# Kernel optimization log

Hardware: AMD Instinct MI355X
Metric: run time of the kernel (lower is better)

Reference implementation:

```python
import jax, jax.numpy as jnp
import numpy as np

B, N_TOK, C = 64, 256, 1024
H = 16
PH, PW = 16, 16  # patch (window) size; N_TOK == PH*PW
D_FF = 4 * C
EPS = 1e-5


def rel_pos_idx(ph, pw):
    # Swin-style relative position index for a ph x pw window -> [ph*pw * ph*pw]
    coords_h = np.arange(ph)
    coords_w = np.arange(pw)
    coords = np.stack(np.meshgrid(coords_h, coords_w, indexing='ij'))  # [2, ph, pw]
    coords = coords.reshape(2, -1)  # [2, N]
    rel = coords[:, :, None] - coords[:, None, :]  # [2, N, N]
    rel = rel.transpose(1, 2, 0)  # [N, N, 2]
    rel[:, :, 0] += ph - 1
    rel[:, :, 1] += pw - 1
    rel[:, :, 0] *= 2 * pw - 1
    return rel.sum(-1).reshape(-1).astype(np.int32)  # [N*N]


def layernorm(x, g, b):
    mu = jnp.mean(x, axis=-1, keepdims=True)
    var = jnp.mean(jnp.square(x - mu), axis=-1, keepdims=True)
    return (x - mu) * jax.lax.rsqrt(var + EPS) * g + b


def setup_inputs() -> dict:
    key = jax.random.key(0)
    ks = jax.random.split(key, 12)
    s = lambda fan: 1.0 / np.sqrt(fan)
    inp = {
        'x': jax.random.normal(ks[0], (B, N_TOK, C), dtype=jnp.float32),
        'rel_pos_idx': jnp.asarray(rel_pos_idx(PH, PW)),
        'qkv_w': jax.random.normal(ks[1], (C, 3 * C), dtype=jnp.float32) * s(C),
        'qkv_b': jnp.zeros((3 * C,), dtype=jnp.float32),
        'proj_w': jax.random.normal(ks[2], (C, C), dtype=jnp.float32) * s(C),
        'proj_b': jnp.zeros((C,), dtype=jnp.float32),
        'rel_pos_bias': jax.random.uniform(ks[3], ((2 * PH - 1) * (2 * PW - 1), H), dtype=jnp.float32),
        'ln1_g': jnp.ones((C,), dtype=jnp.float32),
        'ln1_b': jnp.zeros((C,), dtype=jnp.float32),
        'ln2_g': jnp.ones((C,), dtype=jnp.float32),
        'ln2_b': jnp.zeros((C,), dtype=jnp.float32),
        'fc1_w': jax.random.normal(ks[4], (C, D_FF), dtype=jnp.float32) * s(C),
        'fc1_b': jnp.zeros((D_FF,), dtype=jnp.float32),
        'fc2_w': jax.random.normal(ks[5], (D_FF, C), dtype=jnp.float32) * s(D_FF),
        'fc2_b': jnp.zeros((C,), dtype=jnp.float32),
    }
    return inp


def reference(x, rel_pos_idx, qkv_w, qkv_b, proj_w, proj_b, rel_pos_bias,
              ln1_g, ln1_b, ln2_g, ln2_b, fc1_w, fc1_b, fc2_w, fc2_b):
    Bc, N, Cc = x.shape
    Dh = Cc // H
    scale = Dh ** -0.5

    # --- token mixer: RelAttention with pre-norm residual ---
    h = layernorm(x, ln1_g, ln1_b)
    qkv = (h @ qkv_w + qkv_b).reshape(Bc, N, 3, H, Dh)
    qkv = jnp.transpose(qkv, (2, 0, 3, 1, 4))  # [3, B, H, N, Dh]
    q, k, v = qkv[0] * scale, qkv[1], qkv[2]

    attn = jnp.einsum('bhnd,bhmd->bhnm', q, k)  # [B, H, N, N]
    # gathered relative position bias: [N*N] -> [N, N, H] -> [H, N, N]
    bias = rel_pos_bias[rel_pos_idx].reshape(N, N, H)
    attn = attn + jnp.transpose(bias, (2, 0, 1))[None]
    attn = jax.nn.softmax(attn, axis=-1)

    out = jnp.einsum('bhnm,bhmd->bhnd', attn, v)  # [B, H, N, Dh]
    out = jnp.transpose(out, (0, 2, 1, 3)).reshape(Bc, N, Cc)  # MergeHeads
    x = x + (out @ proj_w + proj_b)

    # --- MLP with pre-norm residual ---
    h2 = layernorm(x, ln2_g, ln2_b)
    h2 = jax.nn.gelu(h2 @ fc1_w + fc1_b)
    x = x + (h2 @ fc2_w + fc2_b)
    return x
```

## Files before the change

### kernel.cpp

```cpp
#include <hip/hip_runtime.h>
#include <hip/hip_bf16.h>
#include <math.h>

typedef __hip_bfloat16 bf16;
typedef __attribute__((ext_vector_type(8))) __bf16 bf16x8;
typedef __attribute__((ext_vector_type(4))) float f32x4;
typedef __attribute__((ext_vector_type(4))) unsigned u32x4;

#define NB 64
#define NTOK 256
#define CDIM 1024
#define NH 16
#define DH 64
#define DFF 4096
#define MROWS (NB * NTOK)

__device__ __forceinline__ float gelu_f(float x) {
    float t = 1.5957691216057308f * (x + 0.044715f * x * x * x);
    return x / (1.0f + __expf(-t));
}

__device__ __forceinline__ void gload_lds16(const void* g, void* l) {
    __builtin_amdgcn_global_load_lds((const __attribute__((address_space(1))) void*)g,
                                     (__attribute__((address_space(3))) void*)l,
                                     16, 0, 0);
}

__global__ void transpose_f32_bf16(const float* __restrict__ in, bf16* __restrict__ out,
                                   int R, int Cc) {
    __shared__ bf16 tile[32][33];
    int c0 = blockIdx.x * 32, r0 = blockIdx.y * 32;
    int t = threadIdx.x;
    int r = t >> 5, c = t & 31;
#pragma unroll
    for (int i = 0; i < 4; i++)
        tile[r + i * 8][c] = (bf16)in[(size_t)(r0 + r + i * 8) * Cc + c0 + c];
    __syncthreads();
#pragma unroll
    for (int i = 0; i < 4; i++)
        out[(size_t)(c0 + r + i * 8) * R + r0 + c] = tile[c][r + i * 8];
}

__global__ __launch_bounds__(256) void ln_kernel(const float* __restrict__ xin,
                                                 const float* __restrict__ g,
                                                 const float* __restrict__ b,
                                                 bf16* __restrict__ outp) {
    __shared__ float red[8];
    int row = blockIdx.x, t = threadIdx.x;
    float4 v = ((const float4*)(xin + (size_t)row * CDIM))[t];
    float s = v.x + v.y + v.z + v.w;
    float q = v.x * v.x + v.y * v.y + v.z * v.z + v.w * v.w;
#pragma unroll
    for (int off = 32; off > 0; off >>= 1) {
        s += __shfl_down(s, off);
        q += __shfl_down(q, off);
    }
    int wave = t >> 6;
    if ((t & 63) == 0) { red[wave] = s; red[4 + wave] = q; }
    __syncthreads();
    float st = red[0] + red[1] + red[2] + red[3];
    float qt = red[4] + red[5] + red[6] + red[7];
    float mu = st * (1.0f / CDIM);
    float rstd = rsqrtf(qt * (1.0f / CDIM) - mu * mu + 1e-5f);
    float4 gv = ((const float4*)g)[t];
    float4 bv = ((const float4*)b)[t];
    bf16* orow = outp + (size_t)row * CDIM + t * 4;
    orow[0] = (bf16)((v.x - mu) * rstd * gv.x + bv.x);
    orow[1] = (bf16)((v.y - mu) * rstd * gv.y + bv.y);
    orow[2] = (bf16)((v.z - mu) * rstd * gv.z + bv.z);
    orow[3] = (bf16)((v.w - mu) * rstd * gv.w + bv.w);
}

__global__ void biasq_kernel(const int* __restrict__ idx, const float* __restrict__ rpb,
                             float* __restrict__ bq) {
    int e = blockIdx.x * 256 + threadIdx.x;
    int k = e & 255, q = (e >> 8) & 255, h = e >> 16;
    bq[e] = rpb[idx[q * 256 + k] * NH + h];
}

__global__ __launch_bounds__(512, 2) void gemm_bt_kernel(
    const bf16* __restrict__ Abf, const bf16* __restrict__ Btbf,
    const float* __restrict__ bias, const float* resid,
    void* outp, size_t qstride, int M, int N, int K, int mode) {
    __shared__ __align__(16) u32x4 SL[4][2][1024];
    const unsigned short* A = (const unsigned short*)Abf;
    const unsigned short* Bt = (const unsigned short*)Btbf;
    int tid = threadIdx.x;
    int wave = tid >> 6, lane = tid & 63;
    int quad = lane >> 4, lr = lane & 15;
    int wm = (wave >> 2) << 7;
    int wn = (wave & 3) << 6;

    unsigned nx = gridDim.x;
    unsigned nwg = nx * gridDim.y;
    unsigned orig = blockIdx.y * nx + blockIdx.x;
    unsigned q8 = nwg >> 3, r8 = nwg & 7u;
    unsigned xcd = orig & 7u, io = orig >> 3;
    unsigned wg = (xcd < r8 ? xcd * (q8 + 1u) : r8 * (q8 + 1u) + (xcd - r8) * q8) + io;
    size_t row0 = (size_t)(wg / nx) << 8;
    size_t col0 = (size_t)(wg % nx) << 8;

    const unsigned short* Ag = A + row0 * K;
    const unsigned short* Bg = Bt + col0 * K;
    f32x4 acc[8][4] = {};

    const int wbase = tid & ~63;

    auto stage = [&](int s) {
        int slot = s & 3;
        int kbase = s << 5;
#pragma unroll
        for (int it = 0; it < 2; it++) {
            int ch = it * 512 + tid;
            int kk = ch >> 8, r = ch & 255;
            gload_lds16(Ag + (size_t)r * K + (kbase + kk * 8),
                        (void*)&SL[slot][0][it * 512 + wbase]);
        }
#pragma unroll
        for (int it = 0; it < 2; it++) {
            int ch = it * 512 + tid;
            int kk = ch >> 8, r = ch & 255;
            gload_lds16(Bg + (size_t)r * K + (kbase + kk * 8),
                        (void*)&SL[slot][1][it * 512 + wbase]);
        }
    };

    int S = K >> 5;
    stage(0);
    stage(1);
    for (int s = 0; s < S; s++) {
        if (s + 2 < S) {
            stage(s + 2);
            asm volatile("s_waitcnt vmcnt(8)" ::: "memory");
        } else if (s + 1 < S) {
            asm volatile("s_waitcnt vmcnt(4)" ::: "memory");
        } else {
            asm volatile("s_waitcnt vmcnt(0)" ::: "memory");
        }
        __builtin_amdgcn_s_barrier();
        asm volatile("" ::: "memory");

        int slot = s & 3;
        bf16x8 bfr[4];
#pragma unroll
        for (int j = 0; j < 4; j++)
            bfr[j] = __builtin_bit_cast(bf16x8, SL[slot][1][quad * 256 + wn + j * 16 + lr]);
#pragma unroll
        for (int ih = 0; ih < 2; ih++) {
            bf16x8 af[4];
#pragma unroll
            for (int i = 0; i < 4; i++)
                af[i] = __builtin_bit_cast(bf16x8,
                    SL[slot][0][quad * 256 + wm + (ih * 4 + i) * 16 + lr]);
            __builtin_amdgcn_s_setprio(1);
#pragma unroll
            for (int i = 0; i < 4; i++)
#pragma unroll
                for (int j = 0; j < 4; j++)
                    acc[ih * 4 + i][j] = __builtin_amdgcn_mfma_f32_16x16x32_bf16(
                        af[i], bfr[j], acc[ih * 4 + i][j], 0, 0, 0);
            __builtin_amdgcn_s_setprio(0);
        }
    }

    float bc[4];
#pragma unroll
    for (int j = 0; j < 4; j++) bc[j] = bias[col0 + wn + j * 16 + lr];
#pragma unroll
    for (int i = 0; i < 8; i++) {
#pragma unroll
        for (int r = 0; r < 4; r++) {
            int R = (int)row0 + wm + i * 16 + quad * 4 + r;
#pragma unroll
            for (int j = 0; j < 4; j++) {
                int Cc = (int)col0 + wn + j * 16 + lr;
                float val = acc[i][j][r] + bc[j];
                if (mode == 0) {
                    int t3 = Cc >> 10, rem = Cc & 1023;
                    int head = rem >> 6, d = rem & 63;
                    int lb = R >> 8, nn = R & 255;
                    if (t3 == 0) val *= 0.125f;
                    ((bf16*)outp)[(size_t)t3 * qstride +
                                  ((size_t)((lb << 4) + head) * NTOK + nn) * DH + d] = (bf16)val;
                } else if (mode == 2) {
                    ((bf16*)outp)[(size_t)R * N + Cc] = (bf16)gelu_f(val);
                } else {
                    val += resid[(size_t)R * N + Cc];
                    ((float*)outp)[(size_t)R * N + Cc] = val;
                }
            }
        }
    }
}

__global__ __launch_bounds__(256, 2) void attn_mfma(
    const bf16* __restrict__ qkv, const float* __restrict__ biasq,
    bf16* __restrict__ outp, size_t qstride) {
    __shared__ u32x4 Ks4[1024];
    __shared__ unsigned Vt32[4096];
    __shared__ u32x4 PQ4[2048];

    int bh = blockIdx.x, lb = bh >> 4, h = bh & 15;
    int tid = threadIdx.x, wave = tid >> 6, lane = tid & 63;
    int quad = lane >> 4, lr = lane & 15;
    int wq = wave << 6;
    const unsigned short* qg = (const unsigned short*)qkv + (size_t)bh * 16384;

    u32x4* pqw = PQ4 + wave * 512;
#pragma unroll
    for (int it = 0; it < 8; it++) {
        int c = it * 64 + lane;
        int qrow = c >> 3, p = c & 7;
        pqw[qrow * 8 + (p ^ (qrow & 7))] =
            *(const u32x4*)(qg + (size_t)(wq + qrow) * 64 + p * 8);
    }
    bf16x8 qf[4][2];
#pragma unroll
    for (int i = 0; i < 4; i++)
#pragma unroll
        for (int ks = 0; ks < 2; ks++) {
            int qrow = i * 16 + lr;
            qf[i][ks] = __builtin_bit_cast(bf16x8,
                pqw[qrow * 8 + (((ks << 2) + quad) ^ (qrow & 7))]);
        }

    f32x4 o[4][4] = {};
    float mrun[4][4], lpart[4][4];
#pragma unroll
    for (int i = 0; i < 4; i++)
#pragma unroll
        for (int r = 0; r < 4; r++) { mrun[i][r] = -1e30f; lpart[i][r] = 0.f; }

    const float* bq = biasq + (size_t)h * 65536;

    for (int half = 0; half < 2; half++) {
        __syncthreads();
        const unsigned short* kg = (const unsigned short*)qkv + qstride +
                                   (size_t)bh * 16384 + half * 8192;
#pragma unroll
        for (int it = 0; it < 4; it++) {
            int c = it * 256 + tid;
            int kr = c >> 3, p = c & 7;
            Ks4[kr * 8 + (p ^ (kr & 7))] = *(const u32x4*)(kg + (size_t)kr * 64 + p * 8);
        }
        const unsigned short* vg = (const unsigned short*)qkv + 2 * qstride +
                                   (size_t)bh * 16384 + half * 8192;
#pragma unroll
        for (int it = 0; it < 16; it++) {
            int idx = it * 256 + tid;
            int d = idx & 63, k2 = idx >> 6;
            unsigned lo = vg[(size_t)(2 * k2) * 64 + d];
            unsigned hi = vg[(size_t)(2 * k2 + 1) * 64 + d];
            int ck = k2 >> 2, w = k2 & 3;
            Vt32[d * 64 + ((ck ^ (d & 15)) << 2) + w] = lo | (hi << 16);
        }
        __syncthreads();

        for (int kb = 0; kb < 2; kb++) {
            f32x4 s[4][4] = {};
#pragma unroll
            for (int ks = 0; ks < 2; ks++) {
                bf16x8 kf[4];
#pragma unroll
                for (int j = 0; j < 4; j++) {
                    int kr = kb * 64 + j * 16 + lr;
                    kf[j] = __builtin_bit_cast(bf16x8,
                        Ks4[kr * 8 + (((ks << 2) + quad) ^ (kr & 7))]);
                }
#pragma unroll
                for (int i = 0; i < 4; i++)
#pragma unroll
                    for (int j = 0; j < 4; j++)
                        s[i][j] = __builtin_amdgcn_mfma_f32_16x16x32_bf16(
                            qf[i][ks], kf[j], s[i][j], 0, 0, 0);
            }
            int kglob = half * 128 + kb * 64;
#pragma unroll
            for (int i = 0; i < 4; i++) {
#pragma unroll
                for (int r = 0; r < 4; r++) {
                    int q = wq + i * 16 + quad * 4 + r;
                    const float* brow = bq + (size_t)q * 256 + kglob + lr;
                    float v0 = s[i][0][r] + brow[0];
                    float v1 = s[i][1][r] + brow[16];
                    float v2 = s[i][2][r] + brow[32];
                    float v3 = s[i][3][r] + brow[48];
                    float mx = fmaxf(fmaxf(v0, v1), fmaxf(v2, v3));
                    mx = fmaxf(mx, __shfl_xor(mx, 1));
                    mx = fmaxf(mx, __shfl_xor(mx, 2));
                    mx = fmaxf(mx, __shfl_xor(mx, 4));
                    mx = fmaxf(mx, __shfl_xor(mx, 8));
                    float mnew = fmaxf(mrun[i][r], mx);
                    float alpha = __expf(mrun[i][r] - mnew);
                    mrun[i][r] = mnew;
                    v0 = __expf(v0 - mnew);
                    v1 = __expf(v1 - mnew);
                    v2 = __expf(v2 - mnew);
                    v3 = __expf(v3 - mnew);
                    lpart[i][r] = lpart[i][r] * alpha + (v0 + v1 + v2 + v3);
                    s[i][0][r] = v0; s[i][1][r] = v1; s[i][2][r] = v2; s[i][3][r] = v3;
#pragma unroll
                    for (int dj = 0; dj < 4; dj++) o[i][dj][r] *= alpha;
                }
            }
            bf16* pqb = (bf16*)pqw;
#pragma unroll
            for (int i = 0; i < 4; i++)
#pragma unroll
                for (int r = 0; r < 4; r++) {
                    int ql = i * 16 + quad * 4 + r;
#pragma unroll
                    for (int j = 0; j < 4; j++) {
                        int col = j * 16 + lr;
                        int ck = col >> 3;
                        pqb[ql * 64 + ((ck ^ (ql & 7)) << 3) + (col & 7)] =
                            (bf16)s[i][j][r];
                    }
                }
            __syncthreads();
#pragma unroll
            for (int ks2 = 0; ks2 < 2; ks2++) {
                bf16x8 pf[4], vf[4];
#pragma unroll
                for (int i = 0; i < 4; i++) {
                    int ql = i * 16 + lr;
                    pf[i] = __builtin_bit_cast(bf16x8,
                        pqw[ql * 8 + (((ks2 << 2) + quad) ^ (ql & 7))]);
                }
#pragma unroll
                for (int dj = 0; dj < 4; dj++) {
                    int d = dj * 16 + lr;
                    int ck = kb * 8 + ks2 * 4 + quad;
                    vf[dj] = __builtin_bit_cast(bf16x8,
                        *(const u32x4*)(Vt32 + d * 64 + ((ck ^ (d & 15)) << 2)));
                }
#pragma unroll
                for (int i = 0; i < 4; i++)
#pragma unroll
                    for (int dj = 0; dj < 4; dj++)
                        o[i][dj] = __builtin_amdgcn_mfma_f32_16x16x32_bf16(
                            pf[i], vf[dj], o[i][dj], 0, 0, 0);
            }
        }
    }

#pragma unroll
    for (int i = 0; i < 4; i++)
#pragma unroll
        for (int r = 0; r < 4; r++) {
            float lp = lpart[i][r];
            lp += __shfl_xor(lp, 1);
            lp += __shfl_xor(lp, 2);
            lp += __shfl_xor(lp, 4);
            lp += __shfl_xor(lp, 8);
            float inv = 1.0f / lp;
            int row = lb * 256 + wq + i * 16 + quad * 4 + r;
            bf16* orow = outp + (size_t)row * CDIM + h * DH;
#pragma unroll
            for (int dj = 0; dj < 4; dj++)
                orow[dj * 16 + lr] = (bf16)(o[i][dj][r] * inv);
        }
}

extern "C" void kernel_launch(void* const* d_in, const int* in_sizes, int n_in,
                              void* d_out, int out_size, void* d_ws, size_t ws_size,
                              hipStream_t stream) {
    const float* x      = (const float*)d_in[0];
    const int*   rpi    = (const int*)d_in[1];
    const float* qkv_w  = (const float*)d_in[2];
    const float* qkv_b  = (const float*)d_in[3];
    const float* proj_w = (const float*)d_in[4];
    const float* proj_b = (const float*)d_in[5];
    const float* rpb    = (const float*)d_in[6];
    const float* ln1g   = (const float*)d_in[7];
    const float* ln1b   = (const float*)d_in[8];
    const float* ln2g   = (const float*)d_in[9];
    const float* ln2b   = (const float*)d_in[10];
    const float* fc1_w  = (const float*)d_in[11];
    const float* fc1_b  = (const float*)d_in[12];
    const float* fc2_w  = (const float*)d_in[13];
    const float* fc2_b  = (const float*)d_in[14];
    float* out = (float*)d_out;
    char* ws = (char*)d_ws;

    bf16* qkvT   = (bf16*)(ws);
    bf16* projT  = (bf16*)(ws + 6291456ull);
    bf16* fc1T   = (bf16*)(ws + 8388608ull);
    bf16* fc2T   = (bf16*)(ws + 16777216ull);
    float* biasq = (float*)(ws + 25165824ull);
    const size_t fixed_end = 29360128ull;

    long long avail = (long long)ws_size - (long long)fixed_end;
    long long rc = avail / 10240;
    rc &= ~255LL;
    if (rc < 256) rc = 256;
    if (rc > MROWS) rc = MROWS;
    const int Rc = (int)rc;
    bf16* hbuf   = (bf16*)(ws + fixed_end);
    bf16* bigbuf = (bf16*)(ws + fixed_end + (size_t)Rc * 2048ull);

    transpose_f32_bf16<<<dim3(3072 / 32, 1024 / 32), 256, 0, stream>>>(qkv_w, qkvT, 1024, 3072);
    transpose_f32_bf16<<<dim3(1024 / 32, 1024 / 32), 256, 0, stream>>>(proj_w, projT, 1024, 1024);
    transpose_f32_bf16<<<dim3(4096 / 32, 1024 / 32), 256, 0, stream>>>(fc1_w, fc1T, 1024, 4096);
    transpose_f32_bf16<<<dim3(1024 / 32, 4096 / 32), 256, 0, stream>>>(fc2_w, fc2T, 4096, 1024);
    biasq_kernel<<<4096, 256, 0, stream>>>(rpi, rpb, biasq);

    for (int r0 = 0; r0 < MROWS; r0 += Rc) {
        int m = MROWS - r0 < Rc ? MROWS - r0 : Rc;
        size_t qs = (size_t)m * 1024;
        ln_kernel<<<m, 256, 0, stream>>>(x + (size_t)r0 * CDIM, ln1g, ln1b, hbuf);
        gemm_bt_kernel<<<dim3(3072 / 256, m / 256), 512, 0, stream>>>(
            hbuf, qkvT, qkv_b, nullptr, bigbuf, qs, m, 3072, 1024, 0);
        attn_mfma<<<(m / 256) * NH, 256, 0, stream>>>(bigbuf, biasq, hbuf, qs);
        gemm_bt_kernel<<<dim3(1024 / 256, m / 256), 512, 0, stream>>>(
            hbuf, projT, proj_b, x + (size_t)r0 * CDIM, out + (size_t)r0 * CDIM, 0,
            m, 1024, 1024, 3);
    }

    for (int r0 = 0; r0 < MROWS; r0 += Rc) {
        int m = MROWS - r0 < Rc ? MROWS - r0 : Rc;
        ln_kernel<<<m, 256, 0, stream>>>(out + (size_t)r0 * CDIM, ln2g, ln2b, hbuf);
        gemm_bt_kernel<<<dim3(4096 / 256, m / 256), 512, 0, stream>>>(
            hbuf, fc1T, fc1_b, nullptr, bigbuf, 0, m, 4096, 1024, 2);
        gemm_bt_kernel<<<dim3(1024 / 256, m / 256), 512, 0, stream>>>(
            bigbuf, fc2T, fc2_b, out + (size_t)r0 * CDIM, out + (size_t)r0 * CDIM, 0,
            m, 1024, 4096, 3);
    }
}
```

Before: 1.244 ms.

## Keep QKV row-major, permute bias table, stage attention output through LDS

The QKV GEMM epilogue now writes a plain row-major [tokens, 3072] tile instead of scattering into a head-major layout, and the attention kernel reads Q/K/V with a 3072-element row stride. The relative-position bias table is permuted so each lane loads its four bias values as one float4. The attention output is staged through LDS so it can be written to global memory as 16-byte vectors, and one block barrier is replaced by a wave-local LDS wait. The aim is to remove scattered 2-byte GEMM stores and uncoalesced bias and output accesses, at the cost of strided reads in attention and reliance on wave-private LDS regions for correctness.

```diff
diff --git a/kernel.cpp b/kernel.cpp
--- a/kernel.cpp
+++ b/kernel.cpp
@@ -74,7 +74,8 @@
 __global__ void biasq_kernel(const int* __restrict__ idx, const float* __restrict__ rpb,
                              float* __restrict__ bq) {
     int e = blockIdx.x * 256 + threadIdx.x;
-    int k = e & 255, q = (e >> 8) & 255, h = e >> 16;
+    int j = e & 3, lr = (e >> 2) & 15, ck = (e >> 6) & 3, q = (e >> 8) & 255, h = e >> 16;
+    int k = ck * 64 + j * 16 + lr;
     bq[e] = rpb[idx[q * 256 + k] * NH + h];
 }
 
@@ -176,12 +177,8 @@
                 int Cc = (int)col0 + wn + j * 16 + lr;
                 float val = acc[i][j][r] + bc[j];
                 if (mode == 0) {
-                    int t3 = Cc >> 10, rem = Cc & 1023;
-                    int head = rem >> 6, d = rem & 63;
-                    int lb = R >> 8, nn = R & 255;
-                    if (t3 == 0) val *= 0.125f;
-                    ((bf16*)outp)[(size_t)t3 * qstride +
-                                  ((size_t)((lb << 4) + head) * NTOK + nn) * DH + d] = (bf16)val;
+                    if (Cc < 1024) val *= 0.125f;
+                    ((bf16*)outp)[(size_t)R * N + Cc] = (bf16)val;
                 } else if (mode == 2) {
                     ((bf16*)outp)[(size_t)R * N + Cc] = (bf16)gelu_f(val);
                 } else {
@@ -204,7 +201,9 @@
     int tid = threadIdx.x, wave = tid >> 6, lane = tid & 63;
     int quad = lane >> 4, lr = lane & 15;
     int wq = wave << 6;
-    const unsigned short* qg = (const unsigned short*)qkv + (size_t)bh * 16384;
+    int tok0 = lb << 8;
+    const unsigned short* base = (const unsigned short*)qkv;
+    const unsigned short* qg = base + (size_t)tok0 * 3072 + h * DH;
 
     u32x4* pqw = PQ4 + wave * 512;
 #pragma unroll
@@ -212,7 +211,7 @@
         int c = it * 64 + lane;
         int qrow = c >> 3, p = c & 7;
         pqw[qrow * 8 + (p ^ (qrow & 7))] =
-            *(const u32x4*)(qg + (size_t)(wq + qrow) * 64 + p * 8);
+            *(const u32x4*)(qg + (size_t)(wq + qrow) * 3072 + p * 8);
     }
     bf16x8 qf[4][2];
 #pragma unroll
@@ -235,22 +234,20 @@
 
     for (int half = 0; half < 2; half++) {
         __syncthreads();
-        const unsigned short* kg = (const unsigned short*)qkv + qstride +
-                                   (size_t)bh * 16384 + half * 8192;
+        const unsigned short* kg = base + (size_t)(tok0 + half * 128) * 3072 + CDIM + h * DH;
 #pragma unroll
         for (int it = 0; it < 4; it++) {
             int c = it * 256 + tid;
             int kr = c >> 3, p = c & 7;
-            Ks4[kr * 8 + (p ^ (kr & 7))] = *(const u32x4*)(kg + (size_t)kr * 64 + p * 8);
-        }
-        const unsigned short* vg = (const unsigned short*)qkv + 2 * qstride +
-                                   (size_t)bh * 16384 + half * 8192;
+            Ks4[kr * 8 + (p ^ (kr & 7))] = *(const u32x4*)(kg + (size_t)kr * 3072 + p * 8);
+        }
+        const unsigned short* vg = base + (size_t)(tok0 + half * 128) * 3072 + 2 * CDIM + h * DH;
 #pragma unroll
         for (int it = 0; it < 16; it++) {
             int idx = it * 256 + tid;
             int d = idx & 63, k2 = idx >> 6;
-            unsigned lo = vg[(size_t)(2 * k2) * 64 + d];
-            unsigned hi = vg[(size_t)(2 * k2 + 1) * 64 + d];
+            unsigned lo = vg[(size_t)(2 * k2) * 3072 + d];
+            unsigned hi = vg[(size_t)(2 * k2 + 1) * 3072 + d];
             int ck = k2 >> 2, w = k2 & 3;
             Vt32[d * 64 + ((ck ^ (d & 15)) << 2) + w] = lo | (hi << 16);
         }
@@ -274,17 +271,17 @@
                         s[i][j] = __builtin_amdgcn_mfma_f32_16x16x32_bf16(
                             qf[i][ks], kf[j], s[i][j], 0, 0, 0);
             }
-            int kglob = half * 128 + kb * 64;
+            int ckb = half * 2 + kb;
 #pragma unroll
             for (int i = 0; i < 4; i++) {
 #pragma unroll
                 for (int r = 0; r < 4; r++) {
                     int q = wq + i * 16 + quad * 4 + r;
-                    const float* brow = bq + (size_t)q * 256 + kglob + lr;
-                    float v0 = s[i][0][r] + brow[0];
-                    float v1 = s[i][1][r] + brow[16];
-                    float v2 = s[i][2][r] + brow[32];
-                    float v3 = s[i][3][r] + brow[48];
+                    float4 bv = *(const float4*)(bq + (size_t)q * 256 + ckb * 64 + lr * 4);
+                    float v0 = s[i][0][r] + bv.x;
+                    float v1 = s[i][1][r] + bv.y;
+                    float v2 = s[i][2][r] + bv.z;
+                    float v3 = s[i][3][r] + bv.w;
                     float mx = fmaxf(fmaxf(v0, v1), fmaxf(v2, v3));
                     mx = fmaxf(mx, __shfl_xor(mx, 1));
                     mx = fmaxf(mx, __shfl_xor(mx, 2));
@@ -317,7 +314,7 @@
                             (bf16)s[i][j][r];
                     }
                 }
-            __syncthreads();
+            asm volatile("s_waitcnt lgkmcnt(0)" ::: "memory");
 #pragma unroll
             for (int ks2 = 0; ks2 < 2; ks2++) {
                 bf16x8 pf[4], vf[4];
@@ -344,6 +341,7 @@
         }
     }
 
+    bf16* ob = (bf16*)pqw;
 #pragma unroll
     for (int i = 0; i < 4; i++)
 #pragma unroll
@@ -354,12 +352,23 @@
             lp += __shfl_xor(lp, 4);
             lp += __shfl_xor(lp, 8);
             float inv = 1.0f / lp;
-            int row = lb * 256 + wq + i * 16 + quad * 4 + r;
-            bf16* orow = outp + (size_t)row * CDIM + h * DH;
-#pragma unroll
-            for (int dj = 0; dj < 4; dj++)
-                orow[dj * 16 + lr] = (bf16)(o[i][dj][r] * inv);
-        }
+            int row = i * 16 + quad * 4 + r;
+#pragma unroll
+            for (int dj = 0; dj < 4; dj++) {
+                int col = dj * 16 + lr;
+                int ck = col >> 3;
+                ob[row * 64 + ((ck ^ (row & 7)) << 3) + (col & 7)] =
+                    (bf16)(o[i][dj][r] * inv);
+            }
+        }
+    asm volatile("s_waitcnt lgkmcnt(0)" ::: "memory");
+#pragma unroll
+    for (int it = 0; it < 8; it++) {
+        int c = it * 64 + lane;
+        int row = c >> 3, p = c & 7;
+        u32x4 v = pqw[row * 8 + (p ^ (row & 7))];
+        *(u32x4*)(outp + (size_t)(tok0 + wq + row) * CDIM + h * DH + p * 8) = v;
+    }
 }
 
 extern "C" void kernel_launch(void* const* d_in, const int* in_sizes, int n_in,
@@ -407,11 +416,10 @@
 
     for (int r0 = 0; r0 < MROWS; r0 += Rc) {
         int m = MROWS - r0 < Rc ? MROWS - r0 : Rc;
-        size_t qs = (size_t)m * 1024;
         ln_kernel<<<m, 256, 0, stream>>>(x + (size_t)r0 * CDIM, ln1g, ln1b, hbuf);
         gemm_bt_kernel<<<dim3(3072 / 256, m / 256), 512, 0, stream>>>(
-            hbuf, qkvT, qkv_b, nullptr, bigbuf, qs, m, 3072, 1024, 0);
-        attn_mfma<<<(m / 256) * NH, 256, 0, stream>>>(bigbuf, biasq, hbuf, qs);
+            hbuf, qkvT, qkv_b, nullptr, bigbuf, 0, m, 3072, 1024, 0);
+        attn_mfma<<<(m / 256) * NH, 256, 0, stream>>>(bigbuf, biasq, hbuf, 0);
         gemm_bt_kernel<<<dim3(1024 / 256, m / 256), 512, 0, stream>>>(
             hbuf, projT, proj_b, x + (size_t)r0 * CDIM, out + (size_t)r0 * CDIM, 0,
             m, 1024, 1024, 3);
```

After: 1.219 ms. -2.0%, faster.
